# Performance work log

Measured on AMD Instinct MI355X. Metric: run time of the kernel, lower is better.

## Reference

```python
import jax, jax.numpy as jnp
import numpy as np

B, S, D, H, DH = 2, 2048, 1024, 16, 64

def setup_inputs() -> dict:
    key = jax.random.key(0)
    ks = jax.random.split(key, 9)
    sc = 0.02
    return {
        "x":  jax.random.normal(ks[0], (B, S, D), jnp.float32),
        "Wq": jax.random.normal(ks[1], (H, D, DH), jnp.float32) * sc,
        "bq": jax.random.normal(ks[2], (H, DH), jnp.float32) * sc,
        "Wk": jax.random.normal(ks[3], (H, D, DH), jnp.float32) * sc,
        "bk": jax.random.normal(ks[4], (H, DH), jnp.float32) * sc,
        "Wv": jax.random.normal(ks[5], (H, D, DH), jnp.float32) * sc,
        "bv": jax.random.normal(ks[6], (H, DH), jnp.float32) * sc,
        "Wo": jax.random.normal(ks[7], (D, D), jnp.float32) * sc,
        "bo": jax.random.normal(ks[8], (D,), jnp.float32) * sc,
    }

def reference(x, Wq, bq, Wk, bk, Wv, bv, Wo, bo):
    # Fused version of the per-head Python loop: all H heads batched.
    # q,k,v: [B,H,S,DH]
    q = jnp.einsum("bsi,hid->bhsd", x, Wq) + bq[None, :, None, :]
    k = jnp.einsum("bsi,hid->bhsd", x, Wk) + bk[None, :, None, :]
    v = jnp.einsum("bsi,hid->bhsd", x, Wv) + bv[None, :, None, :]
    scale = 1.0 / jnp.sqrt(jnp.asarray(DH, x.dtype))
    scores = jnp.einsum("bhsd,bhtd->bhst", q, k) * scale  # [B,H,S,S]
    attn = jax.nn.softmax(scores, axis=-1)
    o = jnp.einsum("bhst,bhtd->bhsd", attn, v)            # [B,H,S,DH]
    # torch.cat([head_0,...,head_{H-1}], dim=-1) -> [B,S,H*DH]
    o = jnp.transpose(o, (0, 2, 1, 3)).reshape(B, S, H * DH)
    # Dropout is identity in eval mode; final dense projection.
    return jnp.einsum("bsi,io->bso", o, Wo) + bo
```

## Files before the change

### kernel.cpp

```cpp
#include <hip/hip_runtime.h>
#include <hip/hip_bf16.h>

#define BB 2
#define SS 2048
#define DD 1024
#define HH 16
#define DHH 64

typedef __attribute__((ext_vector_type(8))) __bf16 bf16x8;
typedef __attribute__((ext_vector_type(4))) float f32x4;
typedef __attribute__((ext_vector_type(16))) float f32x16;
typedef __attribute__((ext_vector_type(4))) int i32x4;
typedef __attribute__((ext_vector_type(4))) unsigned int u32x4;

#define MFMA16 __builtin_amdgcn_mfma_f32_16x16x32_bf16
#define MFMA32 __builtin_amdgcn_mfma_f32_32x32x16_bf16

__device__ __forceinline__ unsigned short f2b(float f) {
  __hip_bfloat16 h = __float2bfloat16(f);
  unsigned short u;
  __builtin_memcpy(&u, &h, 2);
  return u;
}

__device__ __forceinline__ float b2f(unsigned short u) {
  unsigned int x = ((unsigned int)u) << 16;
  float f;
  __builtin_memcpy(&f, &x, 4);
  return f;
}

__device__ __forceinline__ float exp2_fast(float x) {
  float r;
  asm("v_exp_f32 %0, %1" : "=v"(r) : "v"(x));
  return r;
}

__device__ __forceinline__ unsigned int cvtpk_bf16(float lo_, float hi_) {
  unsigned int r;
  asm("v_cvt_pk_bf16_f32 %0, %1, %2" : "=v"(r) : "v"(lo_), "v"(hi_));
  return r;
}

__device__ __forceinline__ void gl_lds16(const void* g, void* l) {
  __builtin_amdgcn_global_load_lds((const __attribute__((address_space(1))) void*)g,
                                   (__attribute__((address_space(3))) void*)l, 16, 0, 0);
}

__global__ __launch_bounds__(256) void k_prep(const float* __restrict__ x,
                                              const float* __restrict__ Wq,
                                              const float* __restrict__ Wk,
                                              const float* __restrict__ Wv,
                                              const float* __restrict__ Wo,
                                              unsigned short* __restrict__ xb,
                                              unsigned short* __restrict__ wqkvt,
                                              unsigned short* __restrict__ wot) {
  int blk = blockIdx.x;
  if (blk < 4096) {
    int i = blk * 256 + threadIdx.x;
    float4 v = ((const float4*)x)[i];
    ushort4 o;
    o.x = f2b(v.x); o.y = f2b(v.y); o.z = f2b(v.z); o.w = f2b(v.w);
    ((ushort4*)xb)[i] = o;
    return;
  }
  __shared__ float t[32][33];
  const float* im;
  unsigned short* om;
  int R, C, c0, r0;
  if (blk < 7168) {
    int bi2 = blk - 4096;
    int z = bi2 >> 6, rem = bi2 & 63;
    im = (z < 16 ? Wq : (z < 32 ? Wk : Wv)) + (size_t)(z & 15) * DD * DHH;
    om = wqkvt + (size_t)z * DD * DHH;
    R = DD; C = DHH;
    c0 = (rem & 1) * 32; r0 = (rem >> 1) * 32;
  } else {
    int bi2 = blk - 7168;
    im = Wo; om = wot;
    R = DD; C = DD;
    c0 = (bi2 & 31) * 32; r0 = (bi2 >> 5) * 32;
  }
  int tx = threadIdx.x & 31, ty = threadIdx.x >> 5;
#pragma unroll
  for (int rr = ty; rr < 32; rr += 8)
    t[rr][tx] = im[(size_t)(r0 + rr) * C + c0 + tx];
  __syncthreads();
#pragma unroll
  for (int rr = ty; rr < 32; rr += 8)
    om[(size_t)(c0 + rr) * R + r0 + tx] = f2b(t[tx][rr]);
}

__global__ __launch_bounds__(256) void k_qkv(const unsigned short* __restrict__ A,
                                             const unsigned short* __restrict__ Wt,
                                             const float* __restrict__ bq,
                                             const float* __restrict__ bk,
                                             const float* __restrict__ bv,
                                             unsigned short* __restrict__ Qb,
                                             unsigned short* __restrict__ Kb,
                                             unsigned short* __restrict__ Vtb) {
  __shared__ __align__(16) unsigned short SMEM[128 * 136];
  unsigned short* As = SMEM;
  unsigned short* Bs = SMEM + 128 * 64;
  int tid = threadIdx.x;
  int w = tid >> 6, l = tid & 63, lr = l & 15, lg = l >> 4;
  int wr = w >> 1, wc = w & 1;
  int col0 = blockIdx.x * 128, row0 = blockIdx.y * 128;
  int sel = col0 >> 10;
  bool vsel = (sel == 2);
  const float* biasp = sel == 0 ? bq : (sel == 1 ? bk : bv);
  unsigned short* outp = sel == 0 ? Qb : Kb;
  float qscale = sel == 0 ? 0.18033688011112042f : 1.0f;

  int r8 = l >> 3, c8 = l & 7;
  const unsigned short* Ab = A + (size_t)(row0 + w * 32 + r8) * DD + c8 * 8;
  const unsigned short* Bb = Wt + (size_t)(col0 + w * 32 + r8) * DD + c8 * 8;

  f32x4 zero = {0.f, 0.f, 0.f, 0.f};
  f32x4 acc[4][4];
#pragma unroll
  for (int m = 0; m < 4; m++)
#pragma unroll
    for (int n = 0; n < 4; n++) acc[m][n] = zero;

  for (int k0 = 0; k0 < DD; k0 += 64) {
    __syncthreads();
#pragma unroll
    for (int c = 0; c < 4; c++) {
      gl_lds16(Ab + (size_t)c * 8 * DD + k0, (char*)As + (w * 32 + c * 8) * 128);
      gl_lds16(Bb + (size_t)c * 8 * DD + k0, (char*)Bs + (w * 32 + c * 8) * 128);
    }
    __syncthreads();
#pragma unroll
    for (int kk = 0; kk < 2; kk++) {
      bf16x8 af[4], bfr[4];
#pragma unroll
      for (int m = 0; m < 4; m++)
        af[m] = *(const bf16x8*)&As[(wr * 64 + m * 16 + lr) * 64 + kk * 32 + lg * 8];
#pragma unroll
      for (int n = 0; n < 4; n++)
        bfr[n] = *(const bf16x8*)&Bs[(wc * 64 + n * 16 + lr) * 64 + kk * 32 + lg * 8];
      if (!vsel) {
#pragma unroll
        for (int m = 0; m < 4; m++)
#pragma unroll
          for (int n = 0; n < 4; n++)
            acc[m][n] = MFMA16(af[m], bfr[n], acc[m][n], 0, 0, 0);
      } else {
#pragma unroll
        for (int m = 0; m < 4; m++)
#pragma unroll
          for (int n = 0; n < 4; n++)
            acc[m][n] = MFMA16(bfr[n], af[m], acc[m][n], 0, 0, 0);
      }
    }
  }

  __syncthreads();
  unsigned short* Ts = SMEM;
  if (!vsel) {
#pragma unroll
    for (int n = 0; n < 4; n++) {
      int cl = wc * 64 + n * 16 + lr;
      float bias = biasp[(col0 + cl) & 1023];
#pragma unroll
      for (int m = 0; m < 4; m++) {
#pragma unroll
        for (int j = 0; j < 4; j++) {
          int sl = wr * 64 + m * 16 + lg * 4 + j;
          Ts[sl * 136 + cl] = f2b((acc[m][n][j] + bias) * qscale);
        }
      }
    }
    __syncthreads();
    int trow = tid >> 4, tc = tid & 15;
#pragma unroll
    for (int pass = 0; pass < 8; pass++) {
      int sl = pass * 16 + trow;
      int c0l = tc * 8;
      i32x4 v = *(const i32x4*)&Ts[sl * 136 + c0l];
      int c = col0 + c0l;
      int hh = (c >> 6) & 15, d = c & 63;
      int row = row0 + sl;
      int b = row >> 11, s = row & 2047;
      *(i32x4*)(outp + ((size_t)(b * HH + hh) * SS + s) * DHH + d) = v;
    }
  } else {
#pragma unroll
    for (int n = 0; n < 4; n++) {
#pragma unroll
      for (int j = 0; j < 4; j++) {
        int cl = wc * 64 + n * 16 + lg * 4 + j;
        float bias = bv[((col0 & 1023) + cl) & 1023];
#pragma unroll
        for (int m = 0; m < 4; m++) {
          int sl = wr * 64 + m * 16 + lr;
          Ts[cl * 136 + sl] = f2b(acc[m][n][j] + bias);
        }
      }
    }
    __syncthreads();
    int trow = tid >> 4, tc = tid & 15;
    int b = row0 >> 11, s0 = row0 & 2047;
#pragma unroll
    for (int pass = 0; pass < 8; pass++) {
      int cl = pass * 16 + trow;
      int s8 = tc * 8;
      i32x4 v = *(const i32x4*)&Ts[cl * 136 + s8];
      int cg = (col0 & 1023) + cl;
      *(i32x4*)(Vtb + (size_t)(b * 1024 + cg) * SS + s0 + s8) = v;
    }
  }
}

__global__ __launch_bounds__(256) void k_proj(const unsigned short* __restrict__ A,
                                              const unsigned short* __restrict__ Wt,
                                              const float* __restrict__ bo,
                                              float* __restrict__ out) {
  __shared__ __align__(16) unsigned short As[128 * 64];
  __shared__ __align__(16) unsigned short Bs[128 * 64];
  int tid = threadIdx.x;
  int w = tid >> 6, l = tid & 63, lr = l & 15, lg = l >> 4;
  int wr = w >> 1, wc = w & 1;
  int col0 = blockIdx.x * 128, row0 = blockIdx.y * 128;

  int r8 = l >> 3, c8 = l & 7;
  const unsigned short* Ab = A + (size_t)(row0 + w * 32 + r8) * DD + c8 * 8;
  const unsigned short* Bb = Wt + (size_t)(col0 + w * 32 + r8) * DD + c8 * 8;

  f32x4 zero = {0.f, 0.f, 0.f, 0.f};
  f32x4 acc[4][4];
#pragma unroll
  for (int m = 0; m < 4; m++)
#pragma unroll
    for (int n = 0; n < 4; n++) acc[m][n] = zero;

  for (int k0 = 0; k0 < DD; k0 += 64) {
    __syncthreads();
#pragma unroll
    for (int c = 0; c < 4; c++) {
      gl_lds16(Ab + (size_t)c * 8 * DD + k0, (char*)As + (w * 32 + c * 8) * 128);
      gl_lds16(Bb + (size_t)c * 8 * DD + k0, (char*)Bs + (w * 32 + c * 8) * 128);
    }
    __syncthreads();
#pragma unroll
    for (int kk = 0; kk < 2; kk++) {
      bf16x8 af[4], bfr[4];
#pragma unroll
      for (int m = 0; m < 4; m++)
        af[m] = *(const bf16x8*)&As[(wr * 64 + m * 16 + lr) * 64 + kk * 32 + lg * 8];
#pragma unroll
      for (int n = 0; n < 4; n++)
        bfr[n] = *(const bf16x8*)&Bs[(wc * 64 + n * 16 + lr) * 64 + kk * 32 + lg * 8];
#pragma unroll
      for (int m = 0; m < 4; m++)
#pragma unroll
        for (int n = 0; n < 4; n++)
          acc[m][n] = MFMA16(af[m], bfr[n], acc[m][n], 0, 0, 0);
    }
  }

#pragma unroll
  for (int n = 0; n < 4; n++) {
    int c = col0 + wc * 64 + n * 16 + lr;
    float bias = bo[c];
#pragma unroll
    for (int m = 0; m < 4; m++) {
#pragma unroll
      for (int j = 0; j < 4; j++) {
        int row = row0 + wr * 64 + m * 16 + lg * 4 + j;
        out[(size_t)row * DD + c] = acc[m][n][j] + bias;
      }
    }
  }
}

#define QT 128
#define KVB 64

__global__ __launch_bounds__(256, 4) void k_attn(const unsigned short* __restrict__ Q,
                                                 const unsigned short* __restrict__ K,
                                                 const unsigned short* __restrict__ Vt,
                                                 unsigned short* __restrict__ Opart,
                                                 float* __restrict__ lse) {
  __shared__ __align__(16) char sm[32768];

  int tid = threadIdx.x;
  int w = tid >> 6, lane = tid & 63;
  int q32 = lane & 31, hi = lane >> 5;
  bool lo = (hi == 0);
  int r8 = lane >> 3, c8 = lane & 7;
  int cg = c8 ^ r8;

  int n = blockIdx.x;
  int bh = ((n & 7) << 2) | ((n >> 3) & 3);
  int rest = n >> 5;
  int q0 = (rest & 15) * QT;
  int chunk = rest >> 4;
  int kvbase = chunk * (SS / 2);

  const unsigned short* Qm = Q + (size_t)bh * SS * DHH;
  const unsigned short* Km = K + (size_t)bh * SS * DHH;
  const unsigned short* Vm = Vt + (size_t)bh * DHH * SS;

  bf16x8 qf[4];
  {
    const unsigned short* qrow = Qm + (size_t)(q0 + w * 32 + q32) * DHH + hi * 8;
#pragma unroll
    for (int ks = 0; ks < 4; ks++)
      qf[ks] = *(const bf16x8*)(qrow + ks * 16);
  }

#pragma unroll
  for (int c = 0; c < 2; c++) {
    int rr = w * 16 + c * 8 + r8;
    gl_lds16(Km + (size_t)(kvbase + rr) * DHH + cg * 8, sm + (w * 16 + c * 8) * 128);
    gl_lds16(Vm + (size_t)rr * SS + kvbase + cg * 8, sm + 16384 + (w * 16 + c * 8) * 128);
  }
  __syncthreads();

  f32x16 oacc0 = {}, oacc1 = {};
  float m_ = -1e30f, l_ = 0.f;
  const int swq = (q32 & 7) << 4;

  for (int t = 0; t < SS / 2 / KVB; t++) {
    const char* Kc = sm + (t & 1) * 8192;
    const char* Vc = sm + 16384 + (t & 1) * 8192;

    if (t + 1 < SS / 2 / KVB) {
      int kv0 = kvbase + (t + 1) * KVB;
      char* kd = sm + ((t + 1) & 1) * 8192;
      char* vd = sm + 16384 + ((t + 1) & 1) * 8192;
#pragma unroll
      for (int c = 0; c < 2; c++) {
        int rr = w * 16 + c * 8 + r8;
        gl_lds16(Km + (size_t)(kv0 + rr) * DHH + cg * 8, kd + (w * 16 + c * 8) * 128);
        gl_lds16(Vm + (size_t)rr * SS + kv0 + cg * 8, vd + (w * 16 + c * 8) * 128);
      }
    }

    f32x16 p0 = {}, p1 = {};
    __builtin_amdgcn_s_setprio(1);
#pragma unroll
    for (int ks = 0; ks < 4; ks++) {
      int co = (ks * 32 + hi * 16) ^ swq;
      bf16x8 kf0 = *(const bf16x8*)(Kc + q32 * 128 + co);
      bf16x8 kf1 = *(const bf16x8*)(Kc + (32 + q32) * 128 + co);
      p0 = MFMA32(kf0, qf[ks], p0, 0, 0, 0);
      p1 = MFMA32(kf1, qf[ks], p1, 0, 0, 0);
    }
    __builtin_amdgcn_s_setprio(0);

    float t8[8];
#pragma unroll
    for (int r = 0; r < 8; r++)
      t8[r] = fmaxf(fmaxf(p0[r], p0[r + 8]), fmaxf(p1[r], p1[r + 8]));
#pragma unroll
    for (int r = 0; r < 4; r++) t8[r] = fmaxf(t8[r], t8[r + 4]);
    float tmax = fmaxf(fmaxf(t8[0], t8[1]), fmaxf(t8[2], t8[3]));
    tmax = fmaxf(tmax, __shfl_xor(tmax, 32));

    if (__any(tmax > m_ + 8.0f)) {
      float nm = fmaxf(m_, tmax);
      float al = exp2_fast(m_ - nm);
      m_ = nm; l_ *= al;
#pragma unroll
      for (int r = 0; r < 16; r++) { oacc0[r] *= al; oacc1[r] *= al; }
    }

#pragma unroll
    for (int r = 0; r < 16; r++) p0[r] = exp2_fast(p0[r] - m_);
#pragma unroll
    for (int r = 0; r < 16; r++) p1[r] = exp2_fast(p1[r] - m_);
    float s8[8];
#pragma unroll
    for (int r = 0; r < 8; r++) s8[r] = (p0[r] + p0[r + 8]) + (p1[r] + p1[r + 8]);
#pragma unroll
    for (int r = 0; r < 4; r++) s8[r] += s8[r + 4];
    l_ += ((s8[0] + s8[1]) + (s8[2] + s8[3]));

    __builtin_amdgcn_s_setprio(1);
    u32x4 pa;
#define MKPA(PB, u) do { \
    unsigned int x0 = cvtpk_bf16(PB[8*(u)+0], PB[8*(u)+1]); \
    unsigned int x1 = cvtpk_bf16(PB[8*(u)+2], PB[8*(u)+3]); \
    unsigned int y0 = cvtpk_bf16(PB[8*(u)+4], PB[8*(u)+5]); \
    unsigned int y1 = cvtpk_bf16(PB[8*(u)+6], PB[8*(u)+7]); \
    unsigned int sx0 = (unsigned int)__shfl_xor((int)x0, 32); \
    unsigned int sx1 = (unsigned int)__shfl_xor((int)x1, 32); \
    unsigned int sy0 = (unsigned int)__shfl_xor((int)y0, 32); \
    unsigned int sy1 = (unsigned int)__shfl_xor((int)y1, 32); \
    pa[0] = lo ? x0 : sy0; pa[1] = lo ? x1 : sy1; \
    pa[2] = lo ? sx0 : y0; pa[3] = lo ? sx1 : y1; \
  } while (0)
#define PVSTEP(s) do { \
    bf16x8 pf = *(bf16x8*)&pa; \
    bf16x8 vf0 = *(const bf16x8*)(Vc + q32 * 128 + (((s) * 32 + hi * 16) ^ swq)); \
    bf16x8 vf1 = *(const bf16x8*)(Vc + (32 + q32) * 128 + (((s) * 32 + hi * 16) ^ swq)); \
    oacc0 = MFMA32(vf0, pf, oacc0, 0, 0, 0); \
    oacc1 = MFMA32(vf1, pf, oacc1, 0, 0, 0); \
  } while (0)
    MKPA(p0, 0); PVSTEP(0);
    MKPA(p0, 1); PVSTEP(1);
    MKPA(p1, 0); PVSTEP(2);
    MKPA(p1, 1); PVSTEP(3);
#undef MKPA
#undef PVSTEP
    __builtin_amdgcn_s_setprio(0);

    __syncthreads();
  }

  l_ += __shfl_xor(l_, 32);
  float invl = 1.0f / l_;
  float lsev = m_ + __log2f(l_);
  __syncthreads();
  unsigned short* Os = (unsigned short*)sm;
  int rowq = w * 32 + q32;
#pragma unroll
  for (int r = 0; r < 16; r++) {
    int d = (r & 3) + 8 * (r >> 2) + 4 * hi;
    Os[rowq * 72 + d] = f2b(oacc0[r] * invl);
    Os[rowq * 72 + 32 + d] = f2b(oacc1[r] * invl);
  }
  if (lo) lse[((size_t)chunk * 32 + bh) * SS + q0 + rowq] = lsev;
  __syncthreads();
#pragma unroll
  for (int i = 0; i < 4; i++) {
    int ci = tid + i * 256;
    int r = ci >> 3, c = ci & 7;
    i32x4 v = *(const i32x4*)&Os[r * 72 + c * 8];
    *(i32x4*)(Opart + (((size_t)chunk * 32 + bh) * SS + q0 + r) * DHH + c * 8) = v;
  }
}

__global__ __launch_bounds__(256) void k_comb(const unsigned short* __restrict__ Opart,
                                              const float* __restrict__ lse,
                                              unsigned short* __restrict__ Ocat) {
  int g = blockIdx.x * 256 + threadIdx.x;
  int row = g >> 3;
  int d8 = (g & 7) * 8;
  int bh = row >> 11, q = row & 2047;
  int bi = bh >> 4, h = bh & 15;
  float e0 = lse[row], e1 = lse[BB * HH * SS + row];
  float mx = fmaxf(e0, e1);
  float w0 = exp2_fast(e0 - mx), w1 = exp2_fast(e1 - mx);
  float inv = 1.0f / (w0 + w1);
  w0 *= inv; w1 *= inv;
  const unsigned short* P0 = Opart + (size_t)row * DHH + d8;
  const unsigned short* P1 = P0 + (size_t)BB * HH * SS * DHH;
  ushort4 a0 = *(const ushort4*)P0, a1 = *(const ushort4*)(P0 + 4);
  ushort4 b0 = *(const ushort4*)P1, b1 = *(const ushort4*)(P1 + 4);
  ushort4 o0, o1;
  o0.x = f2b(w0 * b2f(a0.x) + w1 * b2f(b0.x));
  o0.y = f2b(w0 * b2f(a0.y) + w1 * b2f(b0.y));
  o0.z = f2b(w0 * b2f(a0.z) + w1 * b2f(b0.z));
  o0.w = f2b(w0 * b2f(a0.w) + w1 * b2f(b0.w));
  o1.x = f2b(w0 * b2f(a1.x) + w1 * b2f(b1.x));
  o1.y = f2b(w0 * b2f(a1.y) + w1 * b2f(b1.y));
  o1.z = f2b(w0 * b2f(a1.z) + w1 * b2f(b1.z));
  o1.w = f2b(w0 * b2f(a1.w) + w1 * b2f(b1.w));
  unsigned short* op = Ocat + ((size_t)(bi * SS + q)) * DD + h * DHH + d8;
  *(ushort4*)op = o0;
  *(ushort4*)(op + 4) = o1;
}

extern "C" void kernel_launch(void* const* d_in, const int* in_sizes, int n_in,
                              void* d_out, int out_size, void* d_ws, size_t ws_size,
                              hipStream_t stream) {
  const float* x  = (const float*)d_in[0];
  const float* Wq = (const float*)d_in[1];
  const float* bq = (const float*)d_in[2];
  const float* Wk = (const float*)d_in[3];
  const float* bk = (const float*)d_in[4];
  const float* Wv = (const float*)d_in[5];
  const float* bv = (const float*)d_in[6];
  const float* Wo = (const float*)d_in[7];
  const float* bo = (const float*)d_in[8];
  float* out = (float*)d_out;

  char* ws = (char*)d_ws;
  unsigned short* xb    = (unsigned short*)(ws);
  unsigned short* wqkvt = (unsigned short*)(ws + (size_t)(8u  << 20));
  unsigned short* wot   = (unsigned short*)(ws + (size_t)(14u << 20));
  unsigned short* Qb    = (unsigned short*)(ws + (size_t)(16u << 20));
  unsigned short* Kb    = (unsigned short*)(ws + (size_t)(24u << 20));
  unsigned short* Vt    = (unsigned short*)(ws + (size_t)(32u << 20));
  unsigned short* Ocat  = (unsigned short*)(ws + (size_t)(40u << 20));
  unsigned short* Opart = (unsigned short*)(ws + (size_t)(48u << 20));
  float*          lse   = (float*)(ws + (size_t)(64u << 20));

  k_prep<<<8192, 256, 0, stream>>>(x, Wq, Wk, Wv, Wo, xb, wqkvt, wot);
  k_qkv<<<dim3(3 * DD / 128, BB * SS / 128), 256, 0, stream>>>(xb, wqkvt, bq, bk, bv, Qb, Kb, Vt);
  k_attn<<<dim3(1024), 256, 0, stream>>>(Qb, Kb, Vt, Opart, lse);
  k_comb<<<dim3(2048), 256, 0, stream>>>(Opart, lse, Ocat);
  k_proj<<<dim3(DD / 128, BB * SS / 128), 256, 0, stream>>>(Ocat, wot, bo, out);
}
```

Baseline: 139.2 us.

## Split attention KV range into four chunks and combine four partials

The attention kernel now splits each head's key/value sequence into four chunks instead of two. That doubles the grid to 2048 blocks and raises the launch-bounds occupancy hint from 4 to 5. The combine kernel merges four log-sum-exp weighted partial outputs per row. The workspace is rearranged with aliasing so the larger partial-output buffer fits, reusing regions whose earlier contents are dead by then. The aim is more parallelism and shorter per-block KV loops, at the cost of extra partial-output traffic in the combine step and tighter register limits.

```diff
diff --git a/kernel.cpp b/kernel.cpp
--- a/kernel.cpp
+++ b/kernel.cpp
@@ -277,8 +277,10 @@
 
 #define QT 128
 #define KVB 64
-
-__global__ __launch_bounds__(256, 4) void k_attn(const unsigned short* __restrict__ Q,
+#define NCHUNK 4
+#define CHS (SS / NCHUNK)
+
+__global__ __launch_bounds__(256, 5) void k_attn(const unsigned short* __restrict__ Q,
                                                  const unsigned short* __restrict__ K,
                                                  const unsigned short* __restrict__ Vt,
                                                  unsigned short* __restrict__ Opart,
@@ -297,7 +299,7 @@
   int rest = n >> 5;
   int q0 = (rest & 15) * QT;
   int chunk = rest >> 4;
-  int kvbase = chunk * (SS / 2);
+  int kvbase = chunk * CHS;
 
   const unsigned short* Qm = Q + (size_t)bh * SS * DHH;
   const unsigned short* Km = K + (size_t)bh * SS * DHH;
@@ -323,11 +325,11 @@
   float m_ = -1e30f, l_ = 0.f;
   const int swq = (q32 & 7) << 4;
 
-  for (int t = 0; t < SS / 2 / KVB; t++) {
+  for (int t = 0; t < CHS / KVB; t++) {
     const char* Kc = sm + (t & 1) * 8192;
     const char* Vc = sm + 16384 + (t & 1) * 8192;
 
-    if (t + 1 < SS / 2 / KVB) {
+    if (t + 1 < CHS / KVB) {
       int kv0 = kvbase + (t + 1) * KVB;
       char* kd = sm + ((t + 1) & 1) * 8192;
       char* vd = sm + 16384 + ((t + 1) & 1) * 8192;
@@ -442,24 +444,22 @@
   int d8 = (g & 7) * 8;
   int bh = row >> 11, q = row & 2047;
   int bi = bh >> 4, h = bh & 15;
-  float e0 = lse[row], e1 = lse[BB * HH * SS + row];
-  float mx = fmaxf(e0, e1);
+  const int RS = BB * HH * SS;
+  float e0 = lse[row], e1 = lse[RS + row], e2 = lse[2 * RS + row], e3 = lse[3 * RS + row];
+  float mx = fmaxf(fmaxf(e0, e1), fmaxf(e2, e3));
   float w0 = exp2_fast(e0 - mx), w1 = exp2_fast(e1 - mx);
-  float inv = 1.0f / (w0 + w1);
-  w0 *= inv; w1 *= inv;
+  float w2 = exp2_fast(e2 - mx), w3 = exp2_fast(e3 - mx);
+  float inv = 1.0f / (w0 + w1 + w2 + w3);
+  w0 *= inv; w1 *= inv; w2 *= inv; w3 *= inv;
   const unsigned short* P0 = Opart + (size_t)row * DHH + d8;
-  const unsigned short* P1 = P0 + (size_t)BB * HH * SS * DHH;
-  ushort4 a0 = *(const ushort4*)P0, a1 = *(const ushort4*)(P0 + 4);
-  ushort4 b0 = *(const ushort4*)P1, b1 = *(const ushort4*)(P1 + 4);
+  size_t cs = (size_t)RS * DHH;
+  float o[8];
+#pragma unroll
+  for (int j = 0; j < 8; j++)
+    o[j] = w0 * b2f(P0[j]) + w1 * b2f(P0[cs + j]) + w2 * b2f(P0[2 * cs + j]) + w3 * b2f(P0[3 * cs + j]);
   ushort4 o0, o1;
-  o0.x = f2b(w0 * b2f(a0.x) + w1 * b2f(b0.x));
-  o0.y = f2b(w0 * b2f(a0.y) + w1 * b2f(b0.y));
-  o0.z = f2b(w0 * b2f(a0.z) + w1 * b2f(b0.z));
-  o0.w = f2b(w0 * b2f(a0.w) + w1 * b2f(b0.w));
-  o1.x = f2b(w0 * b2f(a1.x) + w1 * b2f(b1.x));
-  o1.y = f2b(w0 * b2f(a1.y) + w1 * b2f(b1.y));
-  o1.z = f2b(w0 * b2f(a1.z) + w1 * b2f(b1.z));
-  o1.w = f2b(w0 * b2f(a1.w) + w1 * b2f(b1.w));
+  o0.x = f2b(o[0]); o0.y = f2b(o[1]); o0.z = f2b(o[2]); o0.w = f2b(o[3]);
+  o1.x = f2b(o[4]); o1.y = f2b(o[5]); o1.z = f2b(o[6]); o1.w = f2b(o[7]);
   unsigned short* op = Ocat + ((size_t)(bi * SS + q)) * DD + h * DHH + d8;
   *(ushort4*)op = o0;
   *(ushort4*)(op + 4) = o1;
@@ -480,19 +480,19 @@
   float* out = (float*)d_out;
 
   char* ws = (char*)d_ws;
-  unsigned short* xb    = (unsigned short*)(ws);
-  unsigned short* wqkvt = (unsigned short*)(ws + (size_t)(8u  << 20));
-  unsigned short* wot   = (unsigned short*)(ws + (size_t)(14u << 20));
-  unsigned short* Qb    = (unsigned short*)(ws + (size_t)(16u << 20));
-  unsigned short* Kb    = (unsigned short*)(ws + (size_t)(24u << 20));
-  unsigned short* Vt    = (unsigned short*)(ws + (size_t)(32u << 20));
-  unsigned short* Ocat  = (unsigned short*)(ws + (size_t)(40u << 20));
-  unsigned short* Opart = (unsigned short*)(ws + (size_t)(48u << 20));
-  float*          lse   = (float*)(ws + (size_t)(64u << 20));
+  unsigned short* wot   = (unsigned short*)(ws);
+  unsigned short* Qb    = (unsigned short*)(ws + (size_t)(2u  << 20));
+  unsigned short* Kb    = (unsigned short*)(ws + (size_t)(10u << 20));
+  unsigned short* Vt    = (unsigned short*)(ws + (size_t)(18u << 20));
+  unsigned short* Opart = (unsigned short*)(ws + (size_t)(26u << 20));
+  unsigned short* xb    = (unsigned short*)(ws + (size_t)(26u << 20));
+  unsigned short* wqkvt = (unsigned short*)(ws + (size_t)(34u << 20));
+  float*          lse   = (float*)(ws + (size_t)(58u << 20));
+  unsigned short* Ocat  = (unsigned short*)(ws + (size_t)(2u  << 20));
 
   k_prep<<<8192, 256, 0, stream>>>(x, Wq, Wk, Wv, Wo, xb, wqkvt, wot);
   k_qkv<<<dim3(3 * DD / 128, BB * SS / 128), 256, 0, stream>>>(xb, wqkvt, bq, bk, bv, Qb, Kb, Vt);
-  k_attn<<<dim3(1024), 256, 0, stream>>>(Qb, Kb, Vt, Opart, lse);
+  k_attn<<<dim3(2048), 256, 0, stream>>>(Qb, Kb, Vt, Opart, lse);
   k_comb<<<dim3(2048), 256, 0, stream>>>(Opart, lse, Ocat);
   k_proj<<<dim3(DD / 128, BB * SS / 128), 256, 0, stream>>>(Ocat, wot, bo, out);
 }
```

Measured after the change: 158.7 us. +14.0%, slower.

## Fuse split-KV combine into output projection A-tile load

Applied to the files above, without the earlier changes.

Removes the separate combine kernel and the Ocat intermediate buffer. The output projection now reads both partial attention outputs and their LSE values directly, merges them in registers and writes the merged bf16 tile into shared memory as its A operand. This saves one launch and a write plus read of Ocat, but every column block of the projection (8 of them) now recomputes the combine and reads twice the A data. The A load also changes from async global-to-LDS copies to synchronous register loads.

```diff
diff --git a/kernel.cpp b/kernel.cpp
--- a/kernel.cpp
+++ b/kernel.cpp
@@ -6,6 +6,7 @@
 #define DD 1024
 #define HH 16
 #define DHH 64
+#define CHROWS (BB * HH * SS)
 
 typedef __attribute__((ext_vector_type(8))) __bf16 bf16x8;
 typedef __attribute__((ext_vector_type(4))) float f32x4;
@@ -213,7 +214,8 @@
   }
 }
 
-__global__ __launch_bounds__(256) void k_proj(const unsigned short* __restrict__ A,
+__global__ __launch_bounds__(256) void k_proj(const unsigned short* __restrict__ Opart,
+                                              const float* __restrict__ lse,
                                               const unsigned short* __restrict__ Wt,
                                               const float* __restrict__ bo,
                                               float* __restrict__ out) {
@@ -225,8 +227,15 @@
   int col0 = blockIdx.x * 128, row0 = blockIdx.y * 128;
 
   int r8 = l >> 3, c8 = l & 7;
-  const unsigned short* Ab = A + (size_t)(row0 + w * 32 + r8) * DD + c8 * 8;
   const unsigned short* Bb = Wt + (size_t)(col0 + w * 32 + r8) * DD + c8 * 8;
+
+  int bidx[4], sidx[4];
+#pragma unroll
+  for (int c = 0; c < 4; c++) {
+    int grow = row0 + w * 32 + c * 8 + r8;
+    bidx[c] = grow >> 11;
+    sidx[c] = grow & 2047;
+  }
 
   f32x4 zero = {0.f, 0.f, 0.f, 0.f};
   f32x4 acc[4][4];
@@ -236,11 +245,29 @@
     for (int n = 0; n < 4; n++) acc[m][n] = zero;
 
   for (int k0 = 0; k0 < DD; k0 += 64) {
-    __syncthreads();
+    int h = k0 >> 6;
+    __syncthreads();
+#pragma unroll
+    for (int c = 0; c < 4; c++)
+      gl_lds16(Bb + (size_t)c * 8 * DD + k0, (char*)Bs + (w * 32 + c * 8) * 128);
 #pragma unroll
     for (int c = 0; c < 4; c++) {
-      gl_lds16(Ab + (size_t)c * 8 * DD + k0, (char*)As + (w * 32 + c * 8) * 128);
-      gl_lds16(Bb + (size_t)c * 8 * DD + k0, (char*)Bs + (w * 32 + c * 8) * 128);
+      size_t lrow = (size_t)(bidx[c] * HH + h) * SS + sidx[c];
+      float e0 = lse[lrow], e1 = lse[CHROWS + lrow];
+      float mx = fmaxf(e0, e1);
+      float w0 = exp2_fast(e0 - mx), w1 = exp2_fast(e1 - mx);
+      float inv = 1.0f / (w0 + w1);
+      w0 *= inv; w1 *= inv;
+      const unsigned short* p0 = Opart + lrow * DHH + c8 * 8;
+      const unsigned short* p1 = p0 + (size_t)CHROWS * DHH;
+      ushort4 a0 = *(const ushort4*)p0, a1 = *(const ushort4*)(p0 + 4);
+      ushort4 b0 = *(const ushort4*)p1, b1 = *(const ushort4*)(p1 + 4);
+      u32x4 pk;
+      pk[0] = cvtpk_bf16(w0 * b2f(a0.x) + w1 * b2f(b0.x), w0 * b2f(a0.y) + w1 * b2f(b0.y));
+      pk[1] = cvtpk_bf16(w0 * b2f(a0.z) + w1 * b2f(b0.z), w0 * b2f(a0.w) + w1 * b2f(b0.w));
+      pk[2] = cvtpk_bf16(w0 * b2f(a1.x) + w1 * b2f(b1.x), w0 * b2f(a1.y) + w1 * b2f(b1.y));
+      pk[3] = cvtpk_bf16(w0 * b2f(a1.z) + w1 * b2f(b1.z), w0 * b2f(a1.w) + w1 * b2f(b1.w));
+      *(u32x4*)((char*)As + (w * 32 + c * 8 + r8) * 128 + c8 * 16) = pk;
     }
     __syncthreads();
 #pragma unroll
@@ -434,37 +461,6 @@
   }
 }
 
-__global__ __launch_bounds__(256) void k_comb(const unsigned short* __restrict__ Opart,
-                                              const float* __restrict__ lse,
-                                              unsigned short* __restrict__ Ocat) {
-  int g = blockIdx.x * 256 + threadIdx.x;
-  int row = g >> 3;
-  int d8 = (g & 7) * 8;
-  int bh = row >> 11, q = row & 2047;
-  int bi = bh >> 4, h = bh & 15;
-  float e0 = lse[row], e1 = lse[BB * HH * SS + row];
-  float mx = fmaxf(e0, e1);
-  float w0 = exp2_fast(e0 - mx), w1 = exp2_fast(e1 - mx);
-  float inv = 1.0f / (w0 + w1);
-  w0 *= inv; w1 *= inv;
-  const unsigned short* P0 = Opart + (size_t)row * DHH + d8;
-  const unsigned short* P1 = P0 + (size_t)BB * HH * SS * DHH;
-  ushort4 a0 = *(const ushort4*)P0, a1 = *(const ushort4*)(P0 + 4);
-  ushort4 b0 = *(const ushort4*)P1, b1 = *(const ushort4*)(P1 + 4);
-  ushort4 o0, o1;
-  o0.x = f2b(w0 * b2f(a0.x) + w1 * b2f(b0.x));
-  o0.y = f2b(w0 * b2f(a0.y) + w1 * b2f(b0.y));
-  o0.z = f2b(w0 * b2f(a0.z) + w1 * b2f(b0.z));
-  o0.w = f2b(w0 * b2f(a0.w) + w1 * b2f(b0.w));
-  o1.x = f2b(w0 * b2f(a1.x) + w1 * b2f(b1.x));
-  o1.y = f2b(w0 * b2f(a1.y) + w1 * b2f(b1.y));
-  o1.z = f2b(w0 * b2f(a1.z) + w1 * b2f(b1.z));
-  o1.w = f2b(w0 * b2f(a1.w) + w1 * b2f(b1.w));
-  unsigned short* op = Ocat + ((size_t)(bi * SS + q)) * DD + h * DHH + d8;
-  *(ushort4*)op = o0;
-  *(ushort4*)(op + 4) = o1;
-}
-
 extern "C" void kernel_launch(void* const* d_in, const int* in_sizes, int n_in,
                               void* d_out, int out_size, void* d_ws, size_t ws_size,
                               hipStream_t stream) {
@@ -486,13 +482,11 @@
   unsigned short* Qb    = (unsigned short*)(ws + (size_t)(16u << 20));
   unsigned short* Kb    = (unsigned short*)(ws + (size_t)(24u << 20));
   unsigned short* Vt    = (unsigned short*)(ws + (size_t)(32u << 20));
-  unsigned short* Ocat  = (unsigned short*)(ws + (size_t)(40u << 20));
-  unsigned short* Opart = (unsigned short*)(ws + (size_t)(48u << 20));
-  float*          lse   = (float*)(ws + (size_t)(64u << 20));
+  unsigned short* Opart = (unsigned short*)(ws + (size_t)(40u << 20));
+  float*          lse   = (float*)(ws + (size_t)(56u << 20));
 
   k_prep<<<8192, 256, 0, stream>>>(x, Wq, Wk, Wv, Wo, xb, wqkvt, wot);
   k_qkv<<<dim3(3 * DD / 128, BB * SS / 128), 256, 0, stream>>>(xb, wqkvt, bq, bk, bv, Qb, Kb, Vt);
   k_attn<<<dim3(1024), 256, 0, stream>>>(Qb, Kb, Vt, Opart, lse);
-  k_comb<<<dim3(2048), 256, 0, stream>>>(Opart, lse, Ocat);
-  k_proj<<<dim3(DD / 128, BB * SS / 128), 256, 0, stream>>>(Ocat, wot, bo, out);
-}
+  k_proj<<<dim3(DD / 128, BB * SS / 128), 256, 0, stream>>>(Opart, lse, wot, bo, out);
+}
```

After: 151.2 us. +8.7%, slower.
